# Optimization experiments

Hardware: AMD Instinct MI355X
Metric: run time of the kernel (lower is better)

The kernel has to match this reference:

```python
import jax, jax.numpy as jnp
import numpy as np

B, S, HID, H = 2, 2048, 1024, 16
DK = HID // H


def setup_inputs() -> dict:
    key = jax.random.key(0)
    ks = jax.random.split(key, 7)
    x = jax.random.normal(ks[0], (B, S, HID), dtype=jnp.float32)
    mask = jnp.ones((B, 1, 1, S), dtype=jnp.int32)  # padding mask, 1 = keep
    scale = 1.0 / np.sqrt(HID)
    Wq = jax.random.normal(ks[1], (HID, HID), dtype=jnp.float32) * scale
    Wk = jax.random.normal(ks[2], (HID, HID), dtype=jnp.float32) * scale
    Wv = jax.random.normal(ks[3], (HID, HID), dtype=jnp.float32) * scale
    Wo = jax.random.normal(ks[4], (HID, HID), dtype=jnp.float32) * scale
    rel_emb = jax.random.normal(ks[5], (32, H), dtype=jnp.float32) * 0.02
    return {"x": x, "mask": mask, "Wq": Wq, "Wk": Wk, "Wv": Wv, "Wo": Wo, "rel_emb": rel_emb}


def reference(x, mask, Wq, Wk, Wv, Wo, rel_emb):
    bs, seq_len, _ = x.shape
    # nn.Linear(bias=False): y = x @ W.T
    q = (x @ Wq.T).reshape(bs, seq_len, H, DK).transpose(0, 2, 1, 3)  # [B,H,S,D]
    k = (x @ Wk.T).reshape(bs, seq_len, H, DK).transpose(0, 2, 1, 3)
    v = (x @ Wv.T).reshape(bs, seq_len, H, DK).transpose(0, 2, 1, 3)
    scores = jnp.einsum('bhqd,bhkd->bhqk', q, k) / jnp.sqrt(jnp.float32(DK))
    # T5-style clamped relative-position bias
    pos = jnp.arange(seq_len)
    rel = jnp.clip(pos[:, None] - pos[None, :], -16, 15) + 16  # [S,S] in [0,32)
    bias = rel_emb[rel]                      # [S,S,H]
    scores = scores + bias.transpose(2, 0, 1)[None]  # [1,H,S,S]
    # causal mask (is_decoder, self-attention)
    causal = pos[:, None] >= pos[None, :]
    scores = jnp.where(causal[None, None], scores, -jnp.inf)
    # external padding mask
    scores = jnp.where(mask == 0, -jnp.inf, scores)
    attn = jax.nn.softmax(scores, axis=-1)
    attn = jnp.nan_to_num(attn, nan=0.0)     # dropout in eval mode (identity)
    ctx = jnp.einsum('bhqk,bhkd->bhqd', attn, v)
    ctx = ctx.transpose(0, 2, 1, 3).reshape(bs, seq_len, HID)
    return ctx @ Wo.T
```

## Files before the change

### kernel.cpp

```cpp
#include <hip/hip_runtime.h>
#include <math.h>


typedef float    f32x4 __attribute__((ext_vector_type(4)));
typedef _Float16 f16x8 __attribute__((ext_vector_type(8)));
typedef _Float16 f16x4 __attribute__((ext_vector_type(4)));

#define GLD16(gp, lp) __builtin_amdgcn_global_load_lds(                       \
    (const __attribute__((address_space(1))) void*)(gp),                      \
    (__attribute__((address_space(3))) void*)(lp), 16, 0, 0)

static constexpr int kB   = 2;
static constexpr int kS   = 2048;
static constexpr int kHID = 1024;
static constexpr int kH   = 16;

__global__ __launch_bounds__(256) void cvt_f32_f16(const float* __restrict__ src,
                                                   _Float16* __restrict__ dst,
                                                   int n) {
  int i = (blockIdx.x * 256 + threadIdx.x) * 4;
  const int stride = gridDim.x * 256 * 4;
  for (; i < n; i += stride) {
    const float4 v = *reinterpret_cast<const float4*>(src + i);
    f16x4 o;
    o[0] = (_Float16)v.x; o[1] = (_Float16)v.y;
    o[2] = (_Float16)v.z; o[3] = (_Float16)v.w;
    *reinterpret_cast<f16x4*>(dst + i) = o;
  }
}

__global__ __launch_bounds__(256) void cvt_w4(const float* __restrict__ w0,
                                              const float* __restrict__ w1,
                                              const float* __restrict__ w2,
                                              const float* __restrict__ w3,
                                              _Float16* __restrict__ dst) {
  const int wsel = blockIdx.x >> 8;
  const float* src = wsel == 0 ? w0 : wsel == 1 ? w1 : wsel == 2 ? w2 : w3;
  _Float16* d = dst + (long)wsel * 1048576;
  const int base = (blockIdx.x & 255) * 4096;
#pragma unroll
  for (int it = 0; it < 4; ++it) {
    const int i = base + it * 1024 + threadIdx.x * 4;
    const float4 v = *reinterpret_cast<const float4*>(src + i);
    f16x4 o;
    o[0] = (_Float16)v.x; o[1] = (_Float16)v.y;
    o[2] = (_Float16)v.z; o[3] = (_Float16)v.w;
    *reinterpret_cast<f16x4*>(d + i) = o;
  }
}

__global__ __launch_bounds__(256) void prep_mask(const int* __restrict__ maskp,
                                                 float* __restrict__ maskbias,
                                                 unsigned int* __restrict__ tileflags) {
  const int b = blockIdx.x;
  const int tid = threadIdx.x;
  const int wave = tid >> 6, lane = tid & 63;
  __shared__ unsigned int partial[4];
  unsigned int mybits = 0;
#pragma unroll
  for (int it = 0; it < 8; ++it) {
    const int t = it * 4 + wave;
    const int kp = t * 64 + lane;
    const int mv = maskp[b * kS + kp];
    maskbias[b * kS + kp] = mv ? 0.f : -INFINITY;
    const unsigned long long bal = __ballot(mv != 0);
    if (bal == ~0ull) mybits |= (1u << t);
  }
  if (lane == 0) partial[wave] = mybits;
  __syncthreads();
  if (tid == 0) tileflags[b] = partial[0] | partial[1] | partial[2] | partial[3];
}

__global__ __launch_bounds__(256) void gemm_qkv(const _Float16* __restrict__ A,
                                                const _Float16* __restrict__ W,
                                                _Float16* __restrict__ Qh,
                                                _Float16* __restrict__ Kh,
                                                _Float16* __restrict__ Vtg) {
  constexpr int K = kHID;
  __shared__ __align__(16) _Float16 As[128 * 32];
  __shared__ __align__(16) _Float16 Bs[128 * 32];
  const int tid  = threadIdx.x;
  const int lane = tid & 63;
  const int wave = tid >> 6;
  const long bm = (long)blockIdx.y * 128;
  const long bn = (long)blockIdx.x * 128;
  const int wr = (wave >> 1) * 64;
  const int wc = (wave & 1) * 64;

  const int srow = wave * 32 + (lane >> 2);
  const int scol = (lane & 3) * 8;
  const _Float16* ga = A + (bm + srow) * (long)K + scol;
  const _Float16* gb = W + (bn + srow) * (long)K + scol;
  _Float16* lA0 = &As[wave * 1024];
  _Float16* lA1 = &As[wave * 1024 + 512];
  _Float16* lB0 = &Bs[wave * 1024];
  _Float16* lB1 = &Bs[wave * 1024 + 512];

  const int lr = lane & 15;
  const int lk = (lane >> 4) * 8;
  f32x4 acc[4][4] = {};

  for (int k0 = 0; k0 < K; k0 += 32) {
    GLD16(ga + k0, lA0);
    GLD16(ga + k0 + 16 * (long)K, lA1);
    GLD16(gb + k0, lB0);
    GLD16(gb + k0 + 16 * (long)K, lB1);
    __syncthreads();
    f16x8 af[4], bf[4];
#pragma unroll
    for (int i = 0; i < 4; ++i) {
      af[i] = *reinterpret_cast<const f16x8*>(&As[(wr + i * 16 + lr) * 32 + lk]);
      bf[i] = *reinterpret_cast<const f16x8*>(&Bs[(wc + i * 16 + lr) * 32 + lk]);
    }
#pragma unroll
    for (int i = 0; i < 4; ++i)
#pragma unroll
      for (int j = 0; j < 4; ++j)
        acc[i][j] = __builtin_amdgcn_mfma_f32_16x16x32_f16(af[i], bf[j], acc[i][j], 0, 0, 0);
    __syncthreads();
  }

  const int cr0 = wr + (lane >> 4) * 4;
  const int cc0 = wc + lr;
  const int cb = (int)(bn >> 10);
#pragma unroll
  for (int i = 0; i < 4; ++i)
#pragma unroll
    for (int j = 0; j < 4; ++j)
#pragma unroll
      for (int r = 0; r < 4; ++r) {
        const long row = bm + cr0 + i * 16 + r;
        const int  col = (int)bn + cc0 + j * 16;
        const float v = acc[i][j][r];
        if (cb == 0) {
          Qh[row * kHID + col] = (_Float16)(v * 0.125f);
        } else if (cb == 1) {
          Kh[row * kHID + (col - 1024)] = (_Float16)v;
        } else {
          const int hid = col - 2048;
          const int hh = hid >> 6, dd = hid & 63;
          const int bb = (int)(row >> 11), sp = (int)(row & 2047);
          Vtg[((long)(bb * kH + hh) * 64 + dd) * kS + sp] = (_Float16)v;
        }
      }
}

__global__ __launch_bounds__(256) void attn_fwd3(const _Float16* __restrict__ Qh,
                                                 const _Float16* __restrict__ Kh,
                                                 const _Float16* __restrict__ Vtg,
                                                 const float* __restrict__ maskbias,
                                                 const unsigned int* __restrict__ tileflags,
                                                 const float* __restrict__ rel_emb,
                                                 _Float16* __restrict__ ctx) {
  __shared__ __align__(16) _Float16 Kt[2][64 * 64];
  __shared__ __align__(16) _Float16 Vt[2][64 * 64];
  __shared__ float bias_sh[32];

  const int tid  = threadIdx.x;
  const int lane = tid & 63;
  const int wave = tid >> 6;
  const int o = blockIdx.x;
  const int slot = o >> 3;
  const int p = (o & 7) + 8 * (slot >> 4);
  const int qp = slot & 15;
  const int b = p >> 4, h = p & 15;

  const int lr = lane & 15;
  const int lh = lane >> 4;

  if (tid < 32) bias_sh[tid] = rel_emb[tid * kH + h];
  const unsigned int flags = tileflags[b];

  const int srow8  = lane >> 3;
  const int schunk = (lane & 7) ^ srow8;
  const _Float16* ksrc0 = Kh + ((long)b * kS + wave * 16 + srow8) * kHID + h * 64 + schunk * 8;
  const _Float16* ksrc1 = ksrc0 + 8 * kHID;
  const long bh64 = (long)(b * kH + h) * 64;
  const _Float16* vsrc0 = Vtg + (bh64 + wave * 16 + srow8) * kS + schunk * 8;
  const _Float16* vsrc1 = vsrc0 + 8 * kS;

  for (int pass = 0; pass < 2; ++pass) {
    const int qt = (pass == 0) ? qp : 31 - qp;
    const int qbase = qt * 64;

    const long qrow = (long)b * kS + qbase + wave * 16 + lr;
    const f16x8 qf0 = *reinterpret_cast<const f16x8*>(&Qh[qrow * kHID + h * 64 + lh * 8]);
    const f16x8 qf1 = *reinterpret_cast<const f16x8*>(&Qh[qrow * kHID + h * 64 + 32 + lh * 8]);

    float m = -INFINITY, lsum = 0.f;
    f32x4 acco[4] = {};

    GLD16(ksrc0, &Kt[0][wave * 1024]);
    GLD16(ksrc1, &Kt[0][wave * 1024 + 512]);
    GLD16(vsrc0, &Vt[0][wave * 1024]);
    GLD16(vsrc1, &Vt[0][wave * 1024 + 512]);
    __syncthreads();

    const int ntiles = qt + 1;
    for (int kt = 0; kt < ntiles; ++kt) {
      const int cur = kt & 1;
      const int kbase = kt * 64;
      if (kt + 1 < ntiles) {
        GLD16(ksrc0 + (long)(kbase + 64) * kHID, &Kt[cur ^ 1][wave * 1024]);
        GLD16(ksrc1 + (long)(kbase + 64) * kHID, &Kt[cur ^ 1][wave * 1024 + 512]);
        GLD16(vsrc0 + kbase + 64, &Vt[cur ^ 1][wave * 1024]);
        GLD16(vsrc1 + kbase + 64, &Vt[cur ^ 1][wave * 1024 + 512]);
      }
      const char* kb_ = (const char*)&Kt[cur][0];
      const int xa = ((lh ^ (lr & 7)) << 4);
      const int xb = (((4 + lh) ^ (lr & 7)) << 4);
      f32x4 sacc[4] = {};
#pragma unroll
      for (int nb = 0; nb < 4; ++nb) {
        const int rowb = (nb * 16 + lr) * 128;
        const f16x8 kf0 = *reinterpret_cast<const f16x8*>(kb_ + rowb + xa);
        const f16x8 kf1 = *reinterpret_cast<const f16x8*>(kb_ + rowb + xb);
        sacc[nb] = __builtin_amdgcn_mfma_f32_16x16x32_f16(kf0, qf0, sacc[nb], 0, 0, 0);
        sacc[nb] = __builtin_amdgcn_mfma_f32_16x16x32_f16(kf1, qf1, sacc[nb], 0, 0, 0);
      }
      const int q = qbase + wave * 16 + lr;
      const bool tilevalid = (flags >> kt) & 1u;
      float sv[4][4];
      float tmax = -INFINITY;
      if (kt <= qt - 2 && tilevalid) {
        const float b31 = bias_sh[31];
#pragma unroll
        for (int nb = 0; nb < 4; ++nb)
#pragma unroll
          for (int r = 0; r < 4; ++r) {
            sv[nb][r] = sacc[nb][r] + b31;
            tmax = fmaxf(tmax, sv[nb][r]);
          }
      } else {
#pragma unroll
        for (int nb = 0; nb < 4; ++nb)
#pragma unroll
          for (int r = 0; r < 4; ++r) {
            const int kp = kbase + nb * 16 + lh * 4 + r;
            const float mb = tilevalid ? 0.f : maskbias[b * kS + kp];
            int d = q - kp;
            d = d > 15 ? 15 : d;
            d = d < -16 ? -16 : d;
            const float s = sacc[nb][r] + bias_sh[d + 16] + mb;
            sv[nb][r] = (kp <= q) ? s : -INFINITY;
            tmax = fmaxf(tmax, sv[nb][r]);
          }
      }
      tmax = fmaxf(tmax, __shfl_xor(tmax, 16, 64));
      tmax = fmaxf(tmax, __shfl_xor(tmax, 32, 64));
      const float mnew  = fmaxf(m, tmax);
      const float alpha = (mnew == -INFINITY) ? 1.f : __expf(m - mnew);
      float p[4][4];
      float rs = 0.f;
#pragma unroll
      for (int nb = 0; nb < 4; ++nb)
#pragma unroll
        for (int r = 0; r < 4; ++r) {
          const float pv = (sv[nb][r] == -INFINITY) ? 0.f : __expf(sv[nb][r] - mnew);
          p[nb][r] = pv;
          rs += pv;
        }
      rs += __shfl_xor(rs, 16, 64);
      rs += __shfl_xor(rs, 32, 64);
      lsum = lsum * alpha + rs;
      m = mnew;
      float alq[4];
#pragma unroll
      for (int r = 0; r < 4; ++r) alq[r] = __shfl(alpha, lh * 4 + r, 64);
#pragma unroll
      for (int nd = 0; nd < 4; ++nd) {
        acco[nd][0] *= alq[0]; acco[nd][1] *= alq[1];
        acco[nd][2] *= alq[2]; acco[nd][3] *= alq[3];
      }
      int pk[4][2];
#pragma unroll
      for (int nb = 0; nb < 4; ++nb) {
        pk[nb][0] = __builtin_bit_cast(int, __builtin_amdgcn_cvt_pkrtz(p[nb][0], p[nb][1]));
        pk[nb][1] = __builtin_bit_cast(int, __builtin_amdgcn_cvt_pkrtz(p[nb][2], p[nb][3]));
      }
      const int srcA = (((lh * 2) & 3) << 4) | lr;
      const int srcB = (((lh * 2 + 1) & 3) << 4) | lr;
      const bool lo = lh < 2;
      int4 w0, w1;
      {
        int a0 = __shfl(pk[0][0], srcA, 64), b0 = __shfl(pk[1][0], srcA, 64);
        int a1 = __shfl(pk[0][1], srcA, 64), b1 = __shfl(pk[1][1], srcA, 64);
        int a2 = __shfl(pk[0][0], srcB, 64), b2 = __shfl(pk[1][0], srcB, 64);
        int a3 = __shfl(pk[0][1], srcB, 64), b3 = __shfl(pk[1][1], srcB, 64);
        w0.x = lo ? a0 : b0; w0.y = lo ? a1 : b1;
        w0.z = lo ? a2 : b2; w0.w = lo ? a3 : b3;
        a0 = __shfl(pk[2][0], srcA, 64); b0 = __shfl(pk[3][0], srcA, 64);
        a1 = __shfl(pk[2][1], srcA, 64); b1 = __shfl(pk[3][1], srcA, 64);
        a2 = __shfl(pk[2][0], srcB, 64); b2 = __shfl(pk[3][0], srcB, 64);
        a3 = __shfl(pk[2][1], srcB, 64); b3 = __shfl(pk[3][1], srcB, 64);
        w1.x = lo ? a0 : b0; w1.y = lo ? a1 : b1;
        w1.z = lo ? a2 : b2; w1.w = lo ? a3 : b3;
      }
      const f16x8 pa0 = *reinterpret_cast<const f16x8*>(&w0);
      const f16x8 pa1 = *reinterpret_cast<const f16x8*>(&w1);
      const char* vb = (const char*)&Vt[cur][0];
#pragma unroll
      for (int nd = 0; nd < 4; ++nd) {
        const int rowb = (nd * 16 + lr) * 128;
        const f16x8 bv0 = *reinterpret_cast<const f16x8*>(vb + rowb + xa);
        const f16x8 bv1 = *reinterpret_cast<const f16x8*>(vb + rowb + xb);
        acco[nd] = __builtin_amdgcn_mfma_f32_16x16x32_f16(pa0, bv0, acco[nd], 0, 0, 0);
        acco[nd] = __builtin_amdgcn_mfma_f32_16x16x32_f16(pa1, bv1, acco[nd], 0, 0, 0);
      }
      __syncthreads();
    }
    float lsq[4];
#pragma unroll
    for (int r = 0; r < 4; ++r) lsq[r] = __shfl(lsum, lh * 4 + r, 64);
#pragma unroll
    for (int nd = 0; nd < 4; ++nd)
#pragma unroll
      for (int r = 0; r < 4; ++r) {
        const float den = lsq[r];
        const float v = den > 0.f ? acco[nd][r] / den : 0.f;
        ctx[((long)b * kS + qbase + wave * 16 + lh * 4 + r) * kHID + h * 64 + nd * 16 + lr] =
            (_Float16)v;
      }
  }
}

__global__ __launch_bounds__(256) void gemm_out(const _Float16* __restrict__ A,
                                                const _Float16* __restrict__ W,
                                                float* __restrict__ C,
                                                int M, int N, int K) {
  __shared__ __align__(16) _Float16 As[128 * 32];
  __shared__ __align__(16) _Float16 Bs[128 * 32];
  const int tid  = threadIdx.x;
  const int lane = tid & 63;
  const int wave = tid >> 6;
  const long bm = (long)blockIdx.y * 128;
  const long bn = (long)blockIdx.x * 128;
  const int wr = (wave >> 1) * 64;
  const int wc = (wave & 1) * 64;

  const int srow = wave * 32 + (lane >> 2);
  const int scol = (lane & 3) * 8;
  const _Float16* ga = A + (bm + srow) * (long)K + scol;
  const _Float16* gb = W + (bn + srow) * (long)K + scol;
  _Float16* lA0 = &As[wave * 1024];
  _Float16* lA1 = &As[wave * 1024 + 512];
  _Float16* lB0 = &Bs[wave * 1024];
  _Float16* lB1 = &Bs[wave * 1024 + 512];

  const int lr = lane & 15;
  const int lk = (lane >> 4) * 8;
  f32x4 acc[4][4] = {};

  for (int k0 = 0; k0 < K; k0 += 32) {
    GLD16(ga + k0, lA0);
    GLD16(ga + k0 + 16 * (long)K, lA1);
    GLD16(gb + k0, lB0);
    GLD16(gb + k0 + 16 * (long)K, lB1);
    __syncthreads();
    f16x8 af[4], bf[4];
#pragma unroll
    for (int i = 0; i < 4; ++i) {
      af[i] = *reinterpret_cast<const f16x8*>(&As[(wr + i * 16 + lr) * 32 + lk]);
      bf[i] = *reinterpret_cast<const f16x8*>(&Bs[(wc + i * 16 + lr) * 32 + lk]);
    }
#pragma unroll
    for (int i = 0; i < 4; ++i)
#pragma unroll
      for (int j = 0; j < 4; ++j)
        acc[i][j] = __builtin_amdgcn_mfma_f32_16x16x32_f16(af[i], bf[j], acc[i][j], 0, 0, 0);
    __syncthreads();
  }

  const int cr0 = wr + (lane >> 4) * 4;
  const int cc0 = wc + lr;
#pragma unroll
  for (int i = 0; i < 4; ++i)
#pragma unroll
    for (int j = 0; j < 4; ++j)
#pragma unroll
      for (int r = 0; r < 4; ++r)
        C[(bm + cr0 + i * 16 + r) * N + bn + cc0 + j * 16] = acc[i][j][r];
}

extern "C" void kernel_launch(void* const* d_in, const int* in_sizes, int n_in,
                              void* d_out, int out_size, void* d_ws, size_t ws_size,
                              hipStream_t stream) {
  const float* x    = (const float*)d_in[0];
  const int*   mask = (const int*)d_in[1];
  const float* Wq   = (const float*)d_in[2];
  const float* Wk   = (const float*)d_in[3];
  const float* Wv   = (const float*)d_in[4];
  const float* Wo   = (const float*)d_in[5];
  const float* rel  = (const float*)d_in[6];
  float* out = (float*)d_out;

  const int M = kB * kS;
  const int NX = M * kHID;
  const int NW = kHID * kHID;

  _Float16* ws   = (_Float16*)d_ws;
  _Float16* xh   = ws;
  _Float16* wqh  = xh + NX;
  _Float16* woh  = wqh + 3 * NW;
  _Float16* Qh   = woh + NW;
  _Float16* Kh   = Qh + NX;
  _Float16* Vtg  = Kh + NX;
  _Float16* ctxh = Vtg + NX;
  float*        maskbias  = (float*)(ctxh + NX);
  unsigned int* tileflags = (unsigned int*)(maskbias + kB * kS);

  cvt_f32_f16<<<2048, 256, 0, stream>>>(x, xh, NX);
  cvt_w4<<<1024, 256, 0, stream>>>(Wq, Wk, Wv, Wo, wqh);
  prep_mask<<<kB, 256, 0, stream>>>(mask, maskbias, tileflags);

  gemm_qkv<<<dim3(24, 32), 256, 0, stream>>>(xh, wqh, Qh, Kh, Vtg);

  attn_fwd3<<<512, 256, 0, stream>>>(Qh, Kh, Vtg, maskbias, tileflags, rel, ctxh);

  gemm_out<<<dim3(8, 32), 256, 0, stream>>>(ctxh, woh, out, M, kHID, kHID);
}
```

Before: 221.1 us.

## Merge prep kernels, widen attention key tiles, add lazy rescale, shrink out-GEMM tiles

Three prep kernels become one launch. Attention now processes 128-key tiles instead of 64, with a new swizzled V layout. It adds a lazy softmax rescale that skips updating the max when it grows by less than a threshold, and raises wave priority (setprio) around the MFMA blocks. The output GEMM uses 64-row tiles to double the block count. Together these aim to cut launch overhead, loop and barrier overhead, and exp/rescale work, at the cost of more LDS per block and more complex masking conditions.

```diff
diff --git a/kernel.cpp b/kernel.cpp
--- a/kernel.cpp
+++ b/kernel.cpp
@@ -15,60 +15,56 @@
 static constexpr int kHID = 1024;
 static constexpr int kH   = 16;
 
-__global__ __launch_bounds__(256) void cvt_f32_f16(const float* __restrict__ src,
-                                                   _Float16* __restrict__ dst,
-                                                   int n) {
-  int i = (blockIdx.x * 256 + threadIdx.x) * 4;
-  const int stride = gridDim.x * 256 * 4;
-  for (; i < n; i += stride) {
-    const float4 v = *reinterpret_cast<const float4*>(src + i);
-    f16x4 o;
-    o[0] = (_Float16)v.x; o[1] = (_Float16)v.y;
-    o[2] = (_Float16)v.z; o[3] = (_Float16)v.w;
-    *reinterpret_cast<f16x4*>(dst + i) = o;
+__global__ __launch_bounds__(256) void prep_all(const float* __restrict__ x,
+                                                const float* __restrict__ w0,
+                                                const float* __restrict__ w1,
+                                                const float* __restrict__ w2,
+                                                const float* __restrict__ w3,
+                                                const int* __restrict__ maskp,
+                                                _Float16* __restrict__ xh,
+                                                _Float16* __restrict__ wh,
+                                                float* __restrict__ maskbias,
+                                                unsigned int* __restrict__ tileflags) {
+  const int bid = blockIdx.x, tid = threadIdx.x;
+  if (bid < 2048) {
+    const float* src;
+    _Float16* dst;
+    int base;
+    if (bid < 1024) {
+      src = x; dst = xh; base = bid * 4096;
+    } else {
+      const int wsel = (bid - 1024) >> 8;
+      src = wsel == 0 ? w0 : wsel == 1 ? w1 : wsel == 2 ? w2 : w3;
+      dst = wh + (long)wsel * 1048576;
+      base = ((bid - 1024) & 255) * 4096;
+    }
+#pragma unroll
+    for (int it = 0; it < 4; ++it) {
+      const int i = base + it * 1024 + tid * 4;
+      const float4 v = *reinterpret_cast<const float4*>(src + i);
+      f16x4 o;
+      o[0] = (_Float16)v.x; o[1] = (_Float16)v.y;
+      o[2] = (_Float16)v.z; o[3] = (_Float16)v.w;
+      *reinterpret_cast<f16x4*>(dst + i) = o;
+    }
+  } else {
+    const int b = bid - 2048;
+    const int wave = tid >> 6, lane = tid & 63;
+    __shared__ unsigned int partial[4];
+    unsigned int mybits = 0;
+#pragma unroll
+    for (int it = 0; it < 8; ++it) {
+      const int t = it * 4 + wave;
+      const int kp = t * 64 + lane;
+      const int mv = maskp[b * kS + kp];
+      maskbias[b * kS + kp] = mv ? 0.f : -INFINITY;
+      const unsigned long long bal = __ballot(mv != 0);
+      if (bal == ~0ull) mybits |= (1u << t);
+    }
+    if (lane == 0) partial[wave] = mybits;
+    __syncthreads();
+    if (tid == 0) tileflags[b] = partial[0] | partial[1] | partial[2] | partial[3];
   }
-}
-
-__global__ __launch_bounds__(256) void cvt_w4(const float* __restrict__ w0,
-                                              const float* __restrict__ w1,
-                                              const float* __restrict__ w2,
-                                              const float* __restrict__ w3,
-                                              _Float16* __restrict__ dst) {
-  const int wsel = blockIdx.x >> 8;
-  const float* src = wsel == 0 ? w0 : wsel == 1 ? w1 : wsel == 2 ? w2 : w3;
-  _Float16* d = dst + (long)wsel * 1048576;
-  const int base = (blockIdx.x & 255) * 4096;
-#pragma unroll
-  for (int it = 0; it < 4; ++it) {
-    const int i = base + it * 1024 + threadIdx.x * 4;
-    const float4 v = *reinterpret_cast<const float4*>(src + i);
-    f16x4 o;
-    o[0] = (_Float16)v.x; o[1] = (_Float16)v.y;
-    o[2] = (_Float16)v.z; o[3] = (_Float16)v.w;
-    *reinterpret_cast<f16x4*>(d + i) = o;
-  }
-}
-
-__global__ __launch_bounds__(256) void prep_mask(const int* __restrict__ maskp,
-                                                 float* __restrict__ maskbias,
-                                                 unsigned int* __restrict__ tileflags) {
-  const int b = blockIdx.x;
-  const int tid = threadIdx.x;
-  const int wave = tid >> 6, lane = tid & 63;
-  __shared__ unsigned int partial[4];
-  unsigned int mybits = 0;
-#pragma unroll
-  for (int it = 0; it < 8; ++it) {
-    const int t = it * 4 + wave;
-    const int kp = t * 64 + lane;
-    const int mv = maskp[b * kS + kp];
-    maskbias[b * kS + kp] = mv ? 0.f : -INFINITY;
-    const unsigned long long bal = __ballot(mv != 0);
-    if (bal == ~0ull) mybits |= (1u << t);
-  }
-  if (lane == 0) partial[wave] = mybits;
-  __syncthreads();
-  if (tid == 0) tileflags[b] = partial[0] | partial[1] | partial[2] | partial[3];
 }
 
 __global__ __launch_bounds__(256) void gemm_qkv(const _Float16* __restrict__ A,
@@ -145,15 +141,15 @@
       }
 }
 
-__global__ __launch_bounds__(256) void attn_fwd3(const _Float16* __restrict__ Qh,
+__global__ __launch_bounds__(256) void attn_fwd4(const _Float16* __restrict__ Qh,
                                                  const _Float16* __restrict__ Kh,
                                                  const _Float16* __restrict__ Vtg,
                                                  const float* __restrict__ maskbias,
                                                  const unsigned int* __restrict__ tileflags,
                                                  const float* __restrict__ rel_emb,
                                                  _Float16* __restrict__ ctx) {
-  __shared__ __align__(16) _Float16 Kt[2][64 * 64];
-  __shared__ __align__(16) _Float16 Vt[2][64 * 64];
+  __shared__ __align__(16) _Float16 Kt[2][128 * 64];
+  __shared__ __align__(16) _Float16 Vt[2][64 * 128];
   __shared__ float bias_sh[32];
 
   const int tid  = threadIdx.x;
@@ -161,9 +157,9 @@
   const int wave = tid >> 6;
   const int o = blockIdx.x;
   const int slot = o >> 3;
-  const int p = (o & 7) + 8 * (slot >> 4);
+  const int p_ = (o & 7) + 8 * (slot >> 4);
   const int qp = slot & 15;
-  const int b = p >> 4, h = p & 15;
+  const int b = p_ >> 4, h = p_ & 15;
 
   const int lr = lane & 15;
   const int lh = lane >> 4;
@@ -171,13 +167,22 @@
   if (tid < 32) bias_sh[tid] = rel_emb[tid * kH + h];
   const unsigned int flags = tileflags[b];
 
-  const int srow8  = lane >> 3;
-  const int schunk = (lane & 7) ^ srow8;
-  const _Float16* ksrc0 = Kh + ((long)b * kS + wave * 16 + srow8) * kHID + h * 64 + schunk * 8;
-  const _Float16* ksrc1 = ksrc0 + 8 * kHID;
+  const int kro = wave * 32 + (lane >> 3);
+  const int kch = ((lane & 7) ^ (lane >> 3)) * 8;
+  const _Float16* ksrcT[4];
+#pragma unroll
+  for (int t = 0; t < 4; ++t)
+    ksrcT[t] = Kh + ((long)b * kS + kro + t * 8) * kHID + h * 64 + kch;
   const long bh64 = (long)(b * kH + h) * 64;
-  const _Float16* vsrc0 = Vtg + (bh64 + wave * 16 + srow8) * kS + schunk * 8;
-  const _Float16* vsrc1 = vsrc0 + 8 * kS;
+  const _Float16* vsrcT[4];
+#pragma unroll
+  for (int t = 0; t < 4; ++t) {
+    const int d = wave * 16 + t * 4 + (lane >> 4);
+    const int c = (lane & 15) ^ (d & 15);
+    vsrcT[t] = Vtg + (bh64 + d) * kS + c * 8;
+  }
+
+  __syncthreads();
 
   for (int pass = 0; pass < 2; ++pass) {
     const int qt = (pass == 0) ? qp : 31 - qp;
@@ -190,123 +195,157 @@
     float m = -INFINITY, lsum = 0.f;
     f32x4 acco[4] = {};
 
-    GLD16(ksrc0, &Kt[0][wave * 1024]);
-    GLD16(ksrc1, &Kt[0][wave * 1024 + 512]);
-    GLD16(vsrc0, &Vt[0][wave * 1024]);
-    GLD16(vsrc1, &Vt[0][wave * 1024 + 512]);
-    __syncthreads();
-
-    const int ntiles = qt + 1;
+#pragma unroll
+    for (int t = 0; t < 4; ++t) {
+      GLD16(ksrcT[t], &Kt[0][wave * 2048 + t * 512]);
+      GLD16(vsrcT[t], &Vt[0][wave * 2048 + t * 512]);
+    }
+    __syncthreads();
+
+    const int ntiles = (qt >> 1) + 1;
     for (int kt = 0; kt < ntiles; ++kt) {
       const int cur = kt & 1;
-      const int kbase = kt * 64;
+      const int kbase = kt * 128;
       if (kt + 1 < ntiles) {
-        GLD16(ksrc0 + (long)(kbase + 64) * kHID, &Kt[cur ^ 1][wave * 1024]);
-        GLD16(ksrc1 + (long)(kbase + 64) * kHID, &Kt[cur ^ 1][wave * 1024 + 512]);
-        GLD16(vsrc0 + kbase + 64, &Vt[cur ^ 1][wave * 1024]);
-        GLD16(vsrc1 + kbase + 64, &Vt[cur ^ 1][wave * 1024 + 512]);
+#pragma unroll
+        for (int t = 0; t < 4; ++t) {
+          GLD16(ksrcT[t] + (long)(kbase + 128) * kHID, &Kt[cur ^ 1][wave * 2048 + t * 512]);
+          GLD16(vsrcT[t] + kbase + 128, &Vt[cur ^ 1][wave * 2048 + t * 512]);
+        }
       }
       const char* kb_ = (const char*)&Kt[cur][0];
       const int xa = ((lh ^ (lr & 7)) << 4);
       const int xb = (((4 + lh) ^ (lr & 7)) << 4);
-      f32x4 sacc[4] = {};
-#pragma unroll
-      for (int nb = 0; nb < 4; ++nb) {
+      f32x4 sacc[8] = {};
+      __builtin_amdgcn_s_setprio(1);
+#pragma unroll
+      for (int nb = 0; nb < 8; ++nb) {
         const int rowb = (nb * 16 + lr) * 128;
         const f16x8 kf0 = *reinterpret_cast<const f16x8*>(kb_ + rowb + xa);
         const f16x8 kf1 = *reinterpret_cast<const f16x8*>(kb_ + rowb + xb);
         sacc[nb] = __builtin_amdgcn_mfma_f32_16x16x32_f16(kf0, qf0, sacc[nb], 0, 0, 0);
         sacc[nb] = __builtin_amdgcn_mfma_f32_16x16x32_f16(kf1, qf1, sacc[nb], 0, 0, 0);
       }
+      __builtin_amdgcn_s_setprio(0);
+
       const int q = qbase + wave * 16 + lr;
-      const bool tilevalid = (flags >> kt) & 1u;
-      float sv[4][4];
-      float tmax = -INFINITY;
-      if (kt <= qt - 2 && tilevalid) {
+      const bool tilevalid = ((flags >> (2 * kt)) & 3u) == 3u;
+      const bool fast = tilevalid && (kbase + 142 <= qbase);
+
+      if (fast) {
         const float b31 = bias_sh[31];
-#pragma unroll
-        for (int nb = 0; nb < 4; ++nb)
+        float pmax = sacc[0][0];
+#pragma unroll
+        for (int nb = 0; nb < 8; ++nb)
+#pragma unroll
+          for (int r = 0; r < 4; ++r) pmax = fmaxf(pmax, sacc[nb][r]);
+        float mb = m - b31;
+        if (!__all(pmax <= mb + 8.f)) {
+          float tmax = fmaxf(pmax, __shfl_xor(pmax, 16, 64));
+          tmax = fmaxf(tmax, __shfl_xor(tmax, 32, 64));
+          const float mnew = fmaxf(m, tmax + b31);
+          const float alpha = __expf(m - mnew);
+          lsum *= alpha;
+          float alq[4];
+#pragma unroll
+          for (int r = 0; r < 4; ++r) alq[r] = __shfl(alpha, lh * 4 + r, 64);
+#pragma unroll
+          for (int nd = 0; nd < 4; ++nd) {
+            acco[nd][0] *= alq[0]; acco[nd][1] *= alq[1];
+            acco[nd][2] *= alq[2]; acco[nd][3] *= alq[3];
+          }
+          m = mnew;
+          mb = m - b31;
+        }
+        float rs = 0.f;
+#pragma unroll
+        for (int nb = 0; nb < 8; ++nb)
 #pragma unroll
           for (int r = 0; r < 4; ++r) {
-            sv[nb][r] = sacc[nb][r] + b31;
-            tmax = fmaxf(tmax, sv[nb][r]);
+            const float pv = __expf(sacc[nb][r] - mb);
+            sacc[nb][r] = pv;
+            rs += pv;
           }
+        rs += __shfl_xor(rs, 16, 64);
+        rs += __shfl_xor(rs, 32, 64);
+        lsum += rs;
       } else {
-#pragma unroll
-        for (int nb = 0; nb < 4; ++nb)
+        float pmax = -INFINITY;
+#pragma unroll
+        for (int nb = 0; nb < 8; ++nb)
 #pragma unroll
           for (int r = 0; r < 4; ++r) {
             const int kp = kbase + nb * 16 + lh * 4 + r;
-            const float mb = tilevalid ? 0.f : maskbias[b * kS + kp];
+            const float mbv = tilevalid ? 0.f : maskbias[b * kS + kp];
             int d = q - kp;
             d = d > 15 ? 15 : d;
             d = d < -16 ? -16 : d;
-            const float s = sacc[nb][r] + bias_sh[d + 16] + mb;
-            sv[nb][r] = (kp <= q) ? s : -INFINITY;
-            tmax = fmaxf(tmax, sv[nb][r]);
+            const float s = sacc[nb][r] + bias_sh[d + 16] + mbv;
+            sacc[nb][r] = (kp <= q) ? s : -INFINITY;
+            pmax = fmaxf(pmax, sacc[nb][r]);
           }
-      }
-      tmax = fmaxf(tmax, __shfl_xor(tmax, 16, 64));
-      tmax = fmaxf(tmax, __shfl_xor(tmax, 32, 64));
-      const float mnew  = fmaxf(m, tmax);
-      const float alpha = (mnew == -INFINITY) ? 1.f : __expf(m - mnew);
-      float p[4][4];
-      float rs = 0.f;
-#pragma unroll
-      for (int nb = 0; nb < 4; ++nb)
-#pragma unroll
-        for (int r = 0; r < 4; ++r) {
-          const float pv = (sv[nb][r] == -INFINITY) ? 0.f : __expf(sv[nb][r] - mnew);
-          p[nb][r] = pv;
-          rs += pv;
+        if (!__all(pmax <= m + 8.f)) {
+          float tmax = fmaxf(pmax, __shfl_xor(pmax, 16, 64));
+          tmax = fmaxf(tmax, __shfl_xor(tmax, 32, 64));
+          const float mnew = fmaxf(m, tmax);
+          const float alpha = (mnew == -INFINITY) ? 1.f : __expf(m - mnew);
+          lsum *= alpha;
+          float alq[4];
+#pragma unroll
+          for (int r = 0; r < 4; ++r) alq[r] = __shfl(alpha, lh * 4 + r, 64);
+#pragma unroll
+          for (int nd = 0; nd < 4; ++nd) {
+            acco[nd][0] *= alq[0]; acco[nd][1] *= alq[1];
+            acco[nd][2] *= alq[2]; acco[nd][3] *= alq[3];
+          }
+          m = mnew;
         }
-      rs += __shfl_xor(rs, 16, 64);
-      rs += __shfl_xor(rs, 32, 64);
-      lsum = lsum * alpha + rs;
-      m = mnew;
-      float alq[4];
-#pragma unroll
-      for (int r = 0; r < 4; ++r) alq[r] = __shfl(alpha, lh * 4 + r, 64);
-#pragma unroll
-      for (int nd = 0; nd < 4; ++nd) {
-        acco[nd][0] *= alq[0]; acco[nd][1] *= alq[1];
-        acco[nd][2] *= alq[2]; acco[nd][3] *= alq[3];
-      }
-      int pk[4][2];
-#pragma unroll
-      for (int nb = 0; nb < 4; ++nb) {
-        pk[nb][0] = __builtin_bit_cast(int, __builtin_amdgcn_cvt_pkrtz(p[nb][0], p[nb][1]));
-        pk[nb][1] = __builtin_bit_cast(int, __builtin_amdgcn_cvt_pkrtz(p[nb][2], p[nb][3]));
+        float rs = 0.f;
+#pragma unroll
+        for (int nb = 0; nb < 8; ++nb)
+#pragma unroll
+          for (int r = 0; r < 4; ++r) {
+            const float pv = (sacc[nb][r] == -INFINITY) ? 0.f : __expf(sacc[nb][r] - m);
+            sacc[nb][r] = pv;
+            rs += pv;
+          }
+        rs += __shfl_xor(rs, 16, 64);
+        rs += __shfl_xor(rs, 32, 64);
+        lsum += rs;
+      }
+
+      int pk[8][2];
+#pragma unroll
+      for (int nb = 0; nb < 8; ++nb) {
+        pk[nb][0] = __builtin_bit_cast(int, __builtin_amdgcn_cvt_pkrtz(sacc[nb][0], sacc[nb][1]));
+        pk[nb][1] = __builtin_bit_cast(int, __builtin_amdgcn_cvt_pkrtz(sacc[nb][2], sacc[nb][3]));
       }
       const int srcA = (((lh * 2) & 3) << 4) | lr;
       const int srcB = (((lh * 2 + 1) & 3) << 4) | lr;
       const bool lo = lh < 2;
-      int4 w0, w1;
-      {
-        int a0 = __shfl(pk[0][0], srcA, 64), b0 = __shfl(pk[1][0], srcA, 64);
-        int a1 = __shfl(pk[0][1], srcA, 64), b1 = __shfl(pk[1][1], srcA, 64);
-        int a2 = __shfl(pk[0][0], srcB, 64), b2 = __shfl(pk[1][0], srcB, 64);
-        int a3 = __shfl(pk[0][1], srcB, 64), b3 = __shfl(pk[1][1], srcB, 64);
-        w0.x = lo ? a0 : b0; w0.y = lo ? a1 : b1;
-        w0.z = lo ? a2 : b2; w0.w = lo ? a3 : b3;
-        a0 = __shfl(pk[2][0], srcA, 64); b0 = __shfl(pk[3][0], srcA, 64);
-        a1 = __shfl(pk[2][1], srcA, 64); b1 = __shfl(pk[3][1], srcA, 64);
-        a2 = __shfl(pk[2][0], srcB, 64); b2 = __shfl(pk[3][0], srcB, 64);
-        a3 = __shfl(pk[2][1], srcB, 64); b3 = __shfl(pk[3][1], srcB, 64);
-        w1.x = lo ? a0 : b0; w1.y = lo ? a1 : b1;
-        w1.z = lo ? a2 : b2; w1.w = lo ? a3 : b3;
-      }
-      const f16x8 pa0 = *reinterpret_cast<const f16x8*>(&w0);
-      const f16x8 pa1 = *reinterpret_cast<const f16x8*>(&w1);
+      int4 wv[4];
+#pragma unroll
+      for (int s = 0; s < 4; ++s) {
+        const int a0 = __shfl(pk[2 * s][0], srcA, 64), b0 = __shfl(pk[2 * s + 1][0], srcA, 64);
+        const int a1 = __shfl(pk[2 * s][1], srcA, 64), b1 = __shfl(pk[2 * s + 1][1], srcA, 64);
+        const int a2 = __shfl(pk[2 * s][0], srcB, 64), b2 = __shfl(pk[2 * s + 1][0], srcB, 64);
+        const int a3 = __shfl(pk[2 * s][1], srcB, 64), b3 = __shfl(pk[2 * s + 1][1], srcB, 64);
+        wv[s].x = lo ? a0 : b0; wv[s].y = lo ? a1 : b1;
+        wv[s].z = lo ? a2 : b2; wv[s].w = lo ? a3 : b3;
+      }
       const char* vb = (const char*)&Vt[cur][0];
-#pragma unroll
-      for (int nd = 0; nd < 4; ++nd) {
-        const int rowb = (nd * 16 + lr) * 128;
-        const f16x8 bv0 = *reinterpret_cast<const f16x8*>(vb + rowb + xa);
-        const f16x8 bv1 = *reinterpret_cast<const f16x8*>(vb + rowb + xb);
-        acco[nd] = __builtin_amdgcn_mfma_f32_16x16x32_f16(pa0, bv0, acco[nd], 0, 0, 0);
-        acco[nd] = __builtin_amdgcn_mfma_f32_16x16x32_f16(pa1, bv1, acco[nd], 0, 0, 0);
-      }
+      __builtin_amdgcn_s_setprio(1);
+#pragma unroll
+      for (int s = 0; s < 4; ++s) {
+        const f16x8 pa = *reinterpret_cast<const f16x8*>(&wv[s]);
+#pragma unroll
+        for (int nd = 0; nd < 4; ++nd) {
+          const int rowb = (nd * 16 + lr) * 256;
+          const f16x8 bv = *reinterpret_cast<const f16x8*>(vb + rowb + ((((s * 4) + lh) ^ lr) << 4));
+          acco[nd] = __builtin_amdgcn_mfma_f32_16x16x32_f16(pa, bv, acco[nd], 0, 0, 0);
+        }
+      }
+      __builtin_amdgcn_s_setprio(0);
       __syncthreads();
     }
     float lsq[4];
@@ -328,43 +367,43 @@
                                                 const _Float16* __restrict__ W,
                                                 float* __restrict__ C,
                                                 int M, int N, int K) {
-  __shared__ __align__(16) _Float16 As[128 * 32];
+  __shared__ __align__(16) _Float16 As[64 * 32];
   __shared__ __align__(16) _Float16 Bs[128 * 32];
   const int tid  = threadIdx.x;
   const int lane = tid & 63;
   const int wave = tid >> 6;
-  const long bm = (long)blockIdx.y * 128;
+  const long bm = (long)blockIdx.y * 64;
   const long bn = (long)blockIdx.x * 128;
-  const int wr = (wave >> 1) * 64;
+  const int wr = (wave >> 1) * 32;
   const int wc = (wave & 1) * 64;
 
-  const int srow = wave * 32 + (lane >> 2);
+  const int srowA = wave * 16 + (lane >> 2);
+  const int srowB = wave * 32 + (lane >> 2);
   const int scol = (lane & 3) * 8;
-  const _Float16* ga = A + (bm + srow) * (long)K + scol;
-  const _Float16* gb = W + (bn + srow) * (long)K + scol;
-  _Float16* lA0 = &As[wave * 1024];
-  _Float16* lA1 = &As[wave * 1024 + 512];
+  const _Float16* ga = A + (bm + srowA) * (long)K + scol;
+  const _Float16* gb = W + (bn + srowB) * (long)K + scol;
+  _Float16* lA0 = &As[wave * 512];
   _Float16* lB0 = &Bs[wave * 1024];
   _Float16* lB1 = &Bs[wave * 1024 + 512];
 
   const int lr = lane & 15;
   const int lk = (lane >> 4) * 8;
-  f32x4 acc[4][4] = {};
+  f32x4 acc[2][4] = {};
 
   for (int k0 = 0; k0 < K; k0 += 32) {
     GLD16(ga + k0, lA0);
-    GLD16(ga + k0 + 16 * (long)K, lA1);
     GLD16(gb + k0, lB0);
     GLD16(gb + k0 + 16 * (long)K, lB1);
     __syncthreads();
-    f16x8 af[4], bf[4];
-#pragma unroll
-    for (int i = 0; i < 4; ++i) {
+    f16x8 af[2], bf[4];
+#pragma unroll
+    for (int i = 0; i < 2; ++i)
       af[i] = *reinterpret_cast<const f16x8*>(&As[(wr + i * 16 + lr) * 32 + lk]);
-      bf[i] = *reinterpret_cast<const f16x8*>(&Bs[(wc + i * 16 + lr) * 32 + lk]);
-    }
-#pragma unroll
-    for (int i = 0; i < 4; ++i)
+#pragma unroll
+    for (int j = 0; j < 4; ++j)
+      bf[j] = *reinterpret_cast<const f16x8*>(&Bs[(wc + j * 16 + lr) * 32 + lk]);
+#pragma unroll
+    for (int i = 0; i < 2; ++i)
 #pragma unroll
       for (int j = 0; j < 4; ++j)
         acc[i][j] = __builtin_amdgcn_mfma_f32_16x16x32_f16(af[i], bf[j], acc[i][j], 0, 0, 0);
@@ -374,7 +413,7 @@
   const int cr0 = wr + (lane >> 4) * 4;
   const int cc0 = wc + lr;
 #pragma unroll
-  for (int i = 0; i < 4; ++i)
+  for (int i = 0; i < 2; ++i)
 #pragma unroll
     for (int j = 0; j < 4; ++j)
 #pragma unroll
@@ -409,13 +448,12 @@
   float*        maskbias  = (float*)(ctxh + NX);
   unsigned int* tileflags = (unsigned int*)(maskbias + kB * kS);
 
-  cvt_f32_f16<<<2048, 256, 0, stream>>>(x, xh, NX);
-  cvt_w4<<<1024, 256, 0, stream>>>(Wq, Wk, Wv, Wo, wqh);
-  prep_mask<<<kB, 256, 0, stream>>>(mask, maskbias, tileflags);
+  prep_all<<<2050, 256, 0, stream>>>(x, Wq, Wk, Wv, Wo, mask, xh, wqh,
+                                     maskbias, tileflags);
 
   gemm_qkv<<<dim3(24, 32), 256, 0, stream>>>(xh, wqh, Qh, Kh, Vtg);
 
-  attn_fwd3<<<512, 256, 0, stream>>>(Qh, Kh, Vtg, maskbias, tileflags, rel, ctxh);
-
-  gemm_out<<<dim3(8, 32), 256, 0, stream>>>(ctxh, woh, out, M, kHID, kHID);
+  attn_fwd4<<<512, 256, 0, stream>>>(Qh, Kh, Vtg, maskbias, tileflags, rel, ctxh);
+
+  gemm_out<<<dim3(8, 64), 256, 0, stream>>>(ctxh, woh, out, M, kHID, kHID);
 }
```

Result: faster. 201.2 us (-9.0%).
